# Kernel optimization log

Hardware: AMD Instinct MI355X
Metric: run time of the kernel (lower is better)

## Reference

```python
import jax, jax.numpy as jnp
import numpy as np

EPS = 1e-5

def _conv1x1(w, x):
    # w: [out,in], x: [b,in,h,w] -> [b,out,h,w]
    return jnp.einsum('oi,bihw->bohw', w, x)

def _aggregate(resp, persp, t_w, p_w, g_w, z_w, gamma, beta):
    t = _conv1x1(t_w, persp)                      # b,c,h,w
    b, c, h, w = t.shape
    tq = t.reshape(b, c, h * w).transpose(0, 2, 1)            # b,N,c
    p = _conv1x1(p_w, resp).reshape(b, c, -1)                 # b,c,M
    g = _conv1x1(g_w, resp).reshape(b, c, -1).transpose(0, 2, 1)  # b,M,c
    att = jax.nn.softmax(jnp.einsum('bnc,bcm->bnm', tq, p), axis=2)  # b,N,M
    out = jnp.einsum('bnm,bmc->bnc', att, g)                  # b,N,c
    # faithful to torch: .contiguous().view(b,c,h,w) with NO permute
    out = out.reshape(b, c, h, w)
    z = _conv1x1(z_w, out)                                    # b,Cp,h,w
    mean = z.mean(axis=(0, 2, 3), keepdims=True)
    var = z.var(axis=(0, 2, 3), keepdims=True)                # biased (train-mode BN)
    zn = (z - mean) / jnp.sqrt(var + EPS)
    return zn * gamma[None, :, None, None] + beta[None, :, None, None]

def setup_inputs() -> dict:
    key = jax.random.key(0)
    ks = jax.random.split(key, 32)
    Cp, Cr, planes = 256, [64, 256, 512, 1024, 2048], 64
    hw = [48, 48, 24, 12, 6]
    d = {}
    d['perspective'] = jax.random.normal(ks[0], (4, Cp, 48, 48), jnp.float32)
    for i in range(5):
        d[f'response{i}'] = jax.random.normal(ks[1 + i], (4, Cr[i], hw[i], hw[i]), jnp.float32)
    d['t_w'] = jax.random.normal(ks[6], (planes, Cp), jnp.float32) * 0.05
    d['z_w'] = jax.random.normal(ks[7], (Cp, planes), jnp.float32) * 0.05
    for i in range(5):
        d[f'p{i}_w'] = jax.random.normal(ks[8 + 2 * i], (planes, Cr[i]), jnp.float32) * 0.05
        d[f'g{i}_w'] = jax.random.normal(ks[9 + 2 * i], (planes, Cr[i]), jnp.float32) * 0.05
        d[f'bn{i}_g'] = jnp.ones((Cp,), jnp.float32)
        d[f'bn{i}_b'] = jnp.zeros((Cp,), jnp.float32)
    return d

def reference(perspective, response0, response1, response2, response3, response4,
              t_w, z_w,
              p0_w, g0_w, bn0_g, bn0_b,
              p1_w, g1_w, bn1_g, bn1_b,
              p2_w, g2_w, bn2_g, bn2_b,
              p3_w, g3_w, bn3_g, bn3_b,
              p4_w, g4_w, bn4_g, bn4_b):
    resps = [response0, response1, response2, response3, response4]
    ps = [p0_w, p1_w, p2_w, p3_w, p4_w]
    gs = [g0_w, g1_w, g2_w, g3_w, g4_w]
    gms = [bn0_g, bn1_g, bn2_g, bn3_g, bn4_g]
    bts = [bn0_b, bn1_b, bn2_b, bn3_b, bn4_b]
    out = None
    for i in range(5):
        o = _aggregate(resps[i], perspective, t_w, ps[i], gs[i], z_w, gms[i], bts[i])
        out = o if out is None else out + o
    return out
```

## Files before the change

kernel.cpp:

```cpp
#include <hip/hip_runtime.h>
#include <hip/hip_bf16.h>
#include <string.h>

#define BB 4
#define CPc 256
#define NN 2304

typedef __attribute__((ext_vector_type(8))) short bf16x8;
typedef __attribute__((ext_vector_type(4))) float f32x4;

__device__ __forceinline__ short f2b(float x) {
    __hip_bfloat16 h = __float2bfloat16(x);
    return *reinterpret_cast<short*>(&h);
}
__device__ __forceinline__ float b2f16(short v) {
    union { float f; unsigned u; } x;
    x.u = ((unsigned)(unsigned short)v) << 16;
    return x.f;
}

__global__ __launch_bounds__(256) void k_wcvt(
    const float* __restrict__ t_w, const float* __restrict__ z_w,
    const float* p0, const float* p1, const float* p2, const float* p3, const float* p4,
    const float* g0, const float* g1, const float* g2, const float* g3, const float* g4,
    short* __restrict__ TWb, short* __restrict__ ZWb,
    short* __restrict__ WPb, short* __restrict__ WGb) {
    int idx = blockIdx.x * 256 + threadIdx.x;
    if (idx < 16384) { TWb[idx] = f2b(t_w[idx]); return; }
    if (idx < 32768) { ZWb[idx - 16384] = f2b(z_w[idx - 16384]); return; }
    int k = idx - 32768;
    bool isP = k < 249856;
    if (!isP) k -= 249856;
    int i, off;
    if (k < 4096)        { i = 0; off = 0; }
    else if (k < 20480)  { i = 1; off = 4096; }
    else if (k < 53248)  { i = 2; off = 20480; }
    else if (k < 118784) { i = 3; off = 53248; }
    else                 { i = 4; off = 118784; }
    const float* s;
    if (isP) s = (i == 0) ? p0 : (i == 1) ? p1 : (i == 2) ? p2 : (i == 3) ? p3 : p4;
    else     s = (i == 0) ? g0 : (i == 1) ? g1 : (i == 2) ? g2 : (i == 3) ? g3 : g4;
    (isP ? WPb : WGb)[k] = f2b(s[k - off]);
}

__global__ __launch_bounds__(256) void k_conv(
    const float* __restrict__ persp,
    const float* r0, const float* r1, const float* r2, const float* r3, const float* r4,
    const short* __restrict__ TWb, const short* __restrict__ WPb, const short* __restrict__ WGb,
    short* __restrict__ TQb, short* __restrict__ PTb, short* __restrict__ GTb,
    float* __restrict__ PPART, float* __restrict__ GPART) {
    const int CUM[7]  = {0, 144, 288, 432, 504, 552, 584};
    const int CRs[6]  = {256, 64, 256, 512, 1024, 2048};
    const int Mus[6]  = {2304, 2304, 2304, 576, 144, 36};
    const int Mps[6]  = {2304, 2304, 2304, 576, 192, 64};
    const int KSs[6]  = {1, 1, 1, 2, 4, 8};
    const int WOFF[6] = {0, 0, 4096, 20480, 53248, 118784};
    const int POFF[6] = {0, 0, 589824, 1179648, 1327104, 1376256};
    const int PBASE[6] = {0, 0, 0, 0, 294912, 491520};

    __shared__ __align__(16) short s_a[64][72];

    int blk = blockIdx.x, t = threadIdx.x;
    int w = t >> 6, lane = t & 63, lo = lane & 15, quad = lane >> 4;
    int seg = 0;
#pragma unroll
    for (int s_ = 1; s_ <= 5; ++s_) if (blk >= CUM[s_]) seg = s_;
    int Cr = CRs[seg], M = Mus[seg], Mp = Mps[seg], KS = KSs[seg];
    const float* in = (seg == 0) ? persp : (seg == 1) ? r0 : (seg == 2) ? r1 :
                      (seg == 3) ? r2 : (seg == 4) ? r3 : r4;
    const short* wp = (seg == 0) ? TWb : WPb + WOFF[seg];
    const short* wg = WGb + WOFF[seg];
    bool has_g = (seg != 0);
    int local = blk - CUM[seg];
    int mt = Mp >> 6;
    int b = local / (mt * KS);
    int rem = local % (mt * KS);
    int m0 = (rem / KS) * 64;
    int ksi = rem % KS;
    int kLen = Cr / KS, k0 = ksi * kLen;

    int ml = t & 63;
    int ssw = (ml >> 3) & 7;
    bool mvalid = (m0 + ml) < M;
    const float* inB = in + ((size_t)b * Cr) * M + m0 + ml;

    int mrow = w * 16 + lo;
    int rsw = (mrow >> 3) & 7;

    f32x4 accP[4], accG[4];
#pragma unroll
    for (int ct = 0; ct < 4; ++ct) {
        accP[ct] = f32x4{0.f, 0.f, 0.f, 0.f};
        accG[ct] = f32x4{0.f, 0.f, 0.f, 0.f};
    }

    for (int kc = k0; kc < k0 + kLen; kc += 64) {
        __syncthreads();
#pragma unroll
        for (int r = 0; r < 8; ++r) {
            int kp = (t >> 6) + r * 4;
            int q = kp >> 2, l = kp & 3;
            float v0 = 0.f, v1 = 0.f;
            if (mvalid) {
                v0 = inB[(size_t)(kc + 2 * kp) * M];
                v1 = inB[(size_t)(kc + 2 * kp + 1) * M];
            }
            short2 pk; pk.x = f2b(v0); pk.y = f2b(v1);
            *(short2*)&s_a[ml][(q ^ ssw) * 8 + l * 2] = pk;
        }
        __syncthreads();
        const bf16x8 fr0 = *(const bf16x8*)&s_a[mrow][8 * (quad ^ rsw)];
        const bf16x8 fr1 = *(const bf16x8*)&s_a[mrow][8 * ((4 + quad) ^ rsw)];
#pragma unroll
        for (int ct = 0; ct < 4; ++ct) {
            const bf16x8 fp0 = *(const bf16x8*)&wp[(size_t)(ct * 16 + lo) * Cr + kc + quad * 8];
            const bf16x8 fp1 = *(const bf16x8*)&wp[(size_t)(ct * 16 + lo) * Cr + kc + 32 + quad * 8];
            accP[ct] = __builtin_amdgcn_mfma_f32_16x16x32_bf16(fr0, fp0, accP[ct], 0, 0, 0);
            accP[ct] = __builtin_amdgcn_mfma_f32_16x16x32_bf16(fr1, fp1, accP[ct], 0, 0, 0);
            if (has_g) {
                const bf16x8 fg0 = *(const bf16x8*)&wg[(size_t)(ct * 16 + lo) * Cr + kc + quad * 8];
                const bf16x8 fg1 = *(const bf16x8*)&wg[(size_t)(ct * 16 + lo) * Cr + kc + 32 + quad * 8];
                accG[ct] = __builtin_amdgcn_mfma_f32_16x16x32_bf16(fg0, fr0, accG[ct], 0, 0, 0);
                accG[ct] = __builtin_amdgcn_mfma_f32_16x16x32_bf16(fg1, fr1, accG[ct], 0, 0, 0);
            }
        }
    }
    if (KS == 1) {
        short* outP = (seg == 0) ? TQb : PTb + POFF[seg];
        short* outG = GTb + POFF[seg];
        int mP = m0 + w * 16 + quad * 4;
#pragma unroll
        for (int ct = 0; ct < 4; ++ct) {
            int c = ct * 16 + lo;
#pragma unroll
            for (int rg = 0; rg < 4; ++rg)
                outP[((size_t)b * Mp + mP + rg) * 64 + c] = f2b(accP[ct][rg]);
        }
        if (has_g) {
            int mG = m0 + w * 16 + lo;
#pragma unroll
            for (int ct = 0; ct < 4; ++ct) {
                int cG = ct * 16 + quad * 4;
#pragma unroll
                for (int rg = 0; rg < 4; ++rg)
                    outG[((size_t)b * 64 + cG + rg) * Mp + mG] = f2b(accG[ct][rg]);
            }
        }
    } else {
        int NP = 4 * Mp * 64;
        float* pp = PPART + PBASE[seg] + (size_t)ksi * NP;
        float* gp = GPART + PBASE[seg] + (size_t)ksi * NP;
        int mP = m0 + w * 16 + quad * 4;
#pragma unroll
        for (int ct = 0; ct < 4; ++ct) {
            int c = ct * 16 + lo;
#pragma unroll
            for (int rg = 0; rg < 4; ++rg)
                pp[((size_t)b * Mp + mP + rg) * 64 + c] = accP[ct][rg];
        }
        int mG = m0 + w * 16 + lo;
#pragma unroll
        for (int ct = 0; ct < 4; ++ct) {
            int cG = ct * 16 + quad * 4;
#pragma unroll
            for (int rg = 0; rg < 4; ++rg)
                gp[((size_t)b * 64 + cG + rg) * Mp + mG] = accG[ct][rg];
        }
    }
}

__global__ __launch_bounds__(256) void k_cvt(const float* __restrict__ PPART,
                                             const float* __restrict__ GPART,
                                             short* __restrict__ PTb, short* __restrict__ GTb) {
    const int EC[4]    = {0, 147456, 196608, 212992};
    const int KSv[3]   = {2, 4, 8};
    const int PBASEv[3] = {0, 294912, 491520};
    const int POFFv[3] = {1179648, 1327104, 1376256};
    int e = blockIdx.x * 256 + threadIdx.x;
    int sg = (e < EC[1]) ? 0 : (e < EC[2]) ? 1 : 2;
    int rem = e - EC[sg];
    int KS = KSv[sg];
    int NP = (sg == 0) ? 147456 : (sg == 1) ? 49152 : 16384;
    {
        const float* src = PPART + PBASEv[sg] + rem;
        float p = 0.f;
        for (int s = 0; s < KS; ++s) p += src[(size_t)s * NP];
        PTb[POFFv[sg] + rem] = f2b(p);
    }
    {
        const float* src = GPART + PBASEv[sg] + rem;
        float g = 0.f;
        for (int s = 0; s < KS; ++s) g += src[(size_t)s * NP];
        GTb[POFFv[sg] + rem] = f2b(g);
    }
}

__global__ __launch_bounds__(256) void k_attn(const short* __restrict__ tq,
                                              const short* __restrict__ PTb,
                                              const short* __restrict__ GTb,
                                              short* __restrict__ OUTb,
                                              float* __restrict__ PNUM,
                                              float* __restrict__ PL) {
    const int AM[5]    = {2304, 2304, 576, 144, 36};
    const int AMp[5]   = {2304, 2304, 576, 192, 64};
    const int APOFF[5] = {0, 589824, 1179648, 1327104, 1376256};

    __shared__ __align__(16) short s_P[2][32][72];
    __shared__ float s_l[4][32];

    int t = threadIdx.x;
    int bid = blockIdx.x;
    int seg, r, p;
    if (bid < 2304) { seg = bid / 1152; int wi = bid % 1152; p = wi / 288; r = wi % 288; }
    else            { int q = bid - 2304; seg = 2 + q / 288; r = q % 288; p = 0; }
    int b = r / 72;
    int n0 = (r % 72) * 32;
    int M = AM[seg], Mp = AMp[seg];
    const short* pT = PTb + APOFF[seg];
    const short* gT = GTb + APOFF[seg];

    int w = t >> 6, lane = t & 63, lo = lane & 15, quad = lane >> 4;
    bool domask = (M != Mp);
    bool split = (seg < 2);

    int nch_tot = Mp >> 6;
    int c0, c1;
    if (split) { c0 = p * 9; c1 = c0 + 9; }
    else       { c0 = 0; c1 = nch_tot; }

    const short* tqB = tq + ((size_t)b * NN + n0 + lo) * 64 + quad * 8;
    bf16x8 bq[2][2];
#pragma unroll
    for (int i = 0; i < 2; ++i)
#pragma unroll
        for (int h = 0; h < 2; ++h)
            bq[i][h] = *(const bf16x8*)(tqB + i * 16 * 64 + h * 32);

    const short* pA = pT + ((size_t)b * Mp + w * 16 + lo) * 64 + quad * 8;
    const short* gB = gT + ((size_t)b * 64 + w * 16 + lo) * Mp + quad * 8;

    size_t m00 = (size_t)c0 << 6;
    bf16x8 pa0 = *(const bf16x8*)(pA + m00 * 64);
    bf16x8 pa1 = *(const bf16x8*)(pA + m00 * 64 + 32);
    bf16x8 gb0 = *(const bf16x8*)(gB + m00);
    bf16x8 gb1 = *(const bf16x8*)(gB + m00 + 32);

    f32x4 accO[2];
    accO[0] = f32x4{0.f, 0.f, 0.f, 0.f};
    accO[1] = f32x4{0.f, 0.f, 0.f, 0.f};
    float lsum[2] = {0.f, 0.f};

    for (int ch = c0; ch < c1; ++ch) {
        int m0 = ch << 6;
        bf16x8 pa0n, pa1n, gb0n, gb1n;
        bool more = (ch + 1 < c1);
        if (more) {
            size_t mn = (size_t)(m0 + 64);
            pa0n = *(const bf16x8*)(pA + mn * 64);
            pa1n = *(const bf16x8*)(pA + mn * 64 + 32);
            gb0n = *(const bf16x8*)(gB + mn);
            gb1n = *(const bf16x8*)(gB + mn + 32);
        }
        f32x4 S[2];
        S[0] = f32x4{0.f, 0.f, 0.f, 0.f};
        S[0] = __builtin_amdgcn_mfma_f32_16x16x32_bf16(pa0, bq[0][0], S[0], 0, 0, 0);
        S[0] = __builtin_amdgcn_mfma_f32_16x16x32_bf16(pa1, bq[0][1], S[0], 0, 0, 0);
        S[1] = f32x4{0.f, 0.f, 0.f, 0.f};
        S[1] = __builtin_amdgcn_mfma_f32_16x16x32_bf16(pa0, bq[1][0], S[1], 0, 0, 0);
        S[1] = __builtin_amdgcn_mfma_f32_16x16x32_bf16(pa1, bq[1][1], S[1], 0, 0, 0);
        if (domask) {
#pragma unroll
            for (int rg = 0; rg < 4; ++rg) {
                bool oob = (m0 + w * 16 + quad * 4 + rg) >= M;
                if (oob) { S[0][rg] = -1e30f; S[1][rg] = -1e30f; }
            }
        }
        short (*sp)[72] = s_P[ch & 1];
#pragma unroll
        for (int i = 0; i < 2; ++i) {
            short4 pw;
#pragma unroll
            for (int rg = 0; rg < 4; ++rg) {
                float e = __expf(S[i][rg] - 40.f);
                lsum[i] += e;
                ((short*)&pw)[rg] = f2b(e);
            }
            *(short4*)&sp[i * 16 + lo][w * 16 + quad * 4] = pw;
        }
        __syncthreads();
#pragma unroll
        for (int i = 0; i < 2; ++i) {
            const bf16x8 a0 = *(const bf16x8*)&sp[i * 16 + lo][quad * 8];
            const bf16x8 a1 = *(const bf16x8*)&sp[i * 16 + lo][32 + quad * 8];
            accO[i] = __builtin_amdgcn_mfma_f32_16x16x32_bf16(a0, gb0, accO[i], 0, 0, 0);
            accO[i] = __builtin_amdgcn_mfma_f32_16x16x32_bf16(a1, gb1, accO[i], 0, 0, 0);
        }
        if (more) { pa0 = pa0n; pa1 = pa1n; gb0 = gb0n; gb1 = gb1n; }
    }
#pragma unroll
    for (int i = 0; i < 2; ++i) {
        lsum[i] += __shfl_xor(lsum[i], 16, 64);
        lsum[i] += __shfl_xor(lsum[i], 32, 64);
    }
    if (quad == 0) { s_l[w][lo] = lsum[0]; s_l[w][16 + lo] = lsum[1]; }
    __syncthreads();
    if (split) {
        float* np = PNUM + ((size_t)((seg * 4 + p) * 288 + r)) * 2048;
        float* lp = PL + ((size_t)((seg * 4 + p) * 288 + r)) * 32;
#pragma unroll
        for (int i = 0; i < 2; ++i)
#pragma unroll
            for (int rg = 0; rg < 4; ++rg) {
                int n = i * 16 + quad * 4 + rg;
                np[n * 64 + w * 16 + lo] = accO[i][rg];
                if (w == 0 && lo == 0) {
                    float lt = s_l[0][n] + s_l[1][n] + s_l[2][n] + s_l[3][n];
                    lp[n] = lt;
                }
            }
    } else {
        short* outm = OUTb + (size_t)seg * 589824;
#pragma unroll
        for (int i = 0; i < 2; ++i)
#pragma unroll
            for (int rg = 0; rg < 4; ++rg) {
                int n = i * 16 + quad * 4 + rg;
                float lt = s_l[0][n] + s_l[1][n] + s_l[2][n] + s_l[3][n];
                outm[((size_t)b * NN + n0 + n) * 64 + w * 16 + lo] = f2b(accO[i][rg] / lt);
            }
    }
}

__global__ __launch_bounds__(256) void k_comb(const float* __restrict__ PNUM,
                                              const float* __restrict__ PL,
                                              short* __restrict__ OUTb) {
    int e4 = (blockIdx.x * 256 + threadIdx.x) * 4;
    int s = e4 / 589824;
    int rem = e4 % 589824;
    int r = rem / 2048;
    int off = rem % 2048;
    int n = off >> 6;
    float ax = 0.f, ay = 0.f, az = 0.f, aw = 0.f, l = 0.f;
#pragma unroll
    for (int pp = 0; pp < 4; ++pp) {
        size_t blkb = (size_t)((s * 4 + pp) * 288 + r);
        const float4 v = *(const float4*)&PNUM[blkb * 2048 + off];
        ax += v.x; ay += v.y; az += v.z; aw += v.w;
        l += PL[blkb * 32 + n];
    }
    short4 o;
    o.x = f2b(ax / l);
    o.y = f2b(ay / l);
    o.z = f2b(az / l);
    o.w = f2b(aw / l);
    *(short4*)&OUTb[e4] = o;
}

__global__ __launch_bounds__(256) void k_z(const short* __restrict__ OUTb,
                                           const short* __restrict__ ZWb,
                                           short* __restrict__ Zb,
                                           float* __restrict__ PART) {
    __shared__ __align__(16) short s_ut[64][72];
    int t = threadIdx.x;
    int seg = blockIdx.x / 144;
    int r = blockIdx.x % 144;
    int b = r / 36;
    int sp0 = (r % 36) * 64;
    const short* F = OUTb + (size_t)seg * 589824 + (size_t)b * 147456;
    short* z = Zb + (size_t)seg * 2359296 + (size_t)b * 589824;
    float* part = PART + (size_t)(seg * 144 + r) * 512;

    int w = t >> 6, lane = t & 63, lo = lane & 15, quad = lane >> 4;

    bf16x8 af[4][2];
#pragma unroll
    for (int qt = 0; qt < 4; ++qt)
#pragma unroll
        for (int h = 0; h < 2; ++h)
            af[qt][h] = *(const bf16x8*)&ZWb[(size_t)(w * 64 + qt * 16 + lo) * 64 + h * 32 + quad * 8];

#pragma unroll
    for (int rr = 0; rr < 4; ++rr) {
        int idx = t + rr * 256;
        int spl = idx & 63;
        int cp0 = (idx >> 6) << 2;
        short4 pk;
        pk.x = F[(size_t)(cp0 + 0) * 2304 + sp0 + spl];
        pk.y = F[(size_t)(cp0 + 1) * 2304 + sp0 + spl];
        pk.z = F[(size_t)(cp0 + 2) * 2304 + sp0 + spl];
        pk.w = F[(size_t)(cp0 + 3) * 2304 + sp0 + spl];
        *(short4*)&s_ut[spl][cp0] = pk;
    }
    __syncthreads();

    bf16x8 bfr[4][2];
#pragma unroll
    for (int st = 0; st < 4; ++st)
#pragma unroll
        for (int h = 0; h < 2; ++h)
            bfr[st][h] = *(const bf16x8*)&s_ut[st * 16 + lo][h * 32 + quad * 8];

    f32x4 acc[4][4];
#pragma unroll
    for (int qt = 0; qt < 4; ++qt)
#pragma unroll
        for (int st = 0; st < 4; ++st) {
            acc[qt][st] = f32x4{0.f, 0.f, 0.f, 0.f};
            acc[qt][st] = __builtin_amdgcn_mfma_f32_16x16x32_bf16(af[qt][0], bfr[st][0], acc[qt][st], 0, 0, 0);
            acc[qt][st] = __builtin_amdgcn_mfma_f32_16x16x32_bf16(af[qt][1], bfr[st][1], acc[qt][st], 0, 0, 0);
        }

#pragma unroll
    for (int qt = 0; qt < 4; ++qt) {
        float s1[4] = {0.f, 0.f, 0.f, 0.f};
        float s2[4] = {0.f, 0.f, 0.f, 0.f};
        int qb = w * 64 + qt * 16 + quad * 4;
#pragma unroll
        for (int st = 0; st < 4; ++st) {
            int sp = sp0 + st * 16 + lo;
#pragma unroll
            for (int rg = 0; rg < 4; ++rg) {
                float v = acc[qt][st][rg];
                z[(size_t)(qb + rg) * 2304 + sp] = f2b(v);
                s1[rg] += v;
                s2[rg] += v * v;
            }
        }
#pragma unroll
        for (int rg = 0; rg < 4; ++rg) {
            for (int o = 8; o >= 1; o >>= 1) {
                s1[rg] += __shfl_xor(s1[rg], o, 16);
                s2[rg] += __shfl_xor(s2[rg], o, 16);
            }
            if (lo == 0) {
                float2 v2; v2.x = s1[rg]; v2.y = s2[rg];
                *(float2*)&part[(size_t)(qb + rg) * 2] = v2;
            }
        }
    }
}

__global__ __launch_bounds__(256) void k_stats(const float* __restrict__ PART,
                                               float* __restrict__ STATS) {
    int seg = blockIdx.x;
    int q = threadIdx.x;
    const float* p = PART + (size_t)seg * 144 * 512 + q * 2;
    float s1 = 0.f, s2 = 0.f;
#pragma unroll 16
    for (int blk = 0; blk < 144; ++blk) {
        float2 v = *(const float2*)&p[(size_t)blk * 512];
        s1 += v.x; s2 += v.y;
    }
    STATS[seg * 512 + q * 2] = s1;
    STATS[seg * 512 + q * 2 + 1] = s2;
}

__global__ __launch_bounds__(256) void k_final(
    const short* __restrict__ Zb, const float* __restrict__ STATS,
    const float* g0, const float* g1, const float* g2, const float* g3, const float* g4,
    const float* b0, const float* b1, const float* b2, const float* b3, const float* b4,
    float* __restrict__ outp) {
    int idx4 = (blockIdx.x * 256 + threadIdx.x) * 4;
    int q = (idx4 / NN) & 255;
    const float inv = 1.f / (float)(BB * NN);
    float4 o = {0.f, 0.f, 0.f, 0.f};
#pragma unroll
    for (int i = 0; i < 5; ++i) {
        float mean = STATS[i * 512 + q * 2] * inv;
        float var = STATS[i * 512 + q * 2 + 1] * inv - mean * mean;
        float rr = rsqrtf(var + 1e-5f);
        const float* gm = (i == 0) ? g0 : (i == 1) ? g1 : (i == 2) ? g2 : (i == 3) ? g3 : g4;
        const float* bt = (i == 0) ? b0 : (i == 1) ? b1 : (i == 2) ? b2 : (i == 3) ? b3 : b4;
        float sc = rr * gm[q];
        float ofs = bt[q] - mean * sc;
        short4 zv = *(const short4*)&Zb[(size_t)i * 2359296 + idx4];
        o.x += b2f16(zv.x) * sc + ofs;
        o.y += b2f16(zv.y) * sc + ofs;
        o.z += b2f16(zv.z) * sc + ofs;
        o.w += b2f16(zv.w) * sc + ofs;
    }
    *(float4*)&outp[idx4] = o;
}

extern "C" void kernel_launch(void* const* d_in, const int* in_sizes, int n_in,
                              void* d_out, int out_size, void* d_ws, size_t ws_size,
                              hipStream_t stream) {
    const float* persp = (const float*)d_in[0];
    const float* resp[5];
    for (int i = 0; i < 5; ++i) resp[i] = (const float*)d_in[1 + i];
    const float* t_w = (const float*)d_in[6];
    const float* z_w = (const float*)d_in[7];
    const float *p_w[5], *g_w[5], *bng[5], *bnb[5];
    for (int i = 0; i < 5; ++i) {
        p_w[i] = (const float*)d_in[8 + 4 * i];
        g_w[i] = (const float*)d_in[9 + 4 * i];
        bng[i] = (const float*)d_in[10 + 4 * i];
        bnb[i] = (const float*)d_in[11 + 4 * i];
    }
    short* TQb = (short*)d_ws;
    short* TWb = TQb + 589824;
    short* ZWb = TWb + 16384;
    short* WPb = ZWb + 16384;
    short* WGb = WPb + 249856;
    short* PTb = WGb + 249856;
    short* GTb = PTb + 1392640;
    short* Zb  = GTb + 1392640;
    short* OUTb  = (short*)((float*)d_ws + 7852032);
    float* STATS = (float*)d_ws + 7852032 + 2949120;
    float* PPART = STATS + 2560;
    float* GPART = PPART + 622592;
    float* PNUM = (float*)Zb;
    float* PL   = PNUM + 4718592;

    k_wcvt<<<2080, 256, 0, stream>>>(t_w, z_w,
        p_w[0], p_w[1], p_w[2], p_w[3], p_w[4],
        g_w[0], g_w[1], g_w[2], g_w[3], g_w[4],
        TWb, ZWb, WPb, WGb);
    k_conv<<<584, 256, 0, stream>>>(persp,
        resp[0], resp[1], resp[2], resp[3], resp[4],
        TWb, WPb, WGb, TQb, PTb, GTb, PPART, GPART);
    k_cvt<<<832, 256, 0, stream>>>(PPART, GPART, PTb, GTb);
    k_attn<<<3168, 256, 0, stream>>>(TQb, PTb, GTb, OUTb, PNUM, PL);
    k_comb<<<1152, 256, 0, stream>>>(PNUM, PL, OUTb);
    k_z<<<720, 256, 0, stream>>>(OUTb, ZWb, Zb, PPART);
    k_stats<<<5, 256, 0, stream>>>(PPART, STATS);
    k_final<<<2304, 256, 0, stream>>>(Zb, STATS,
        bng[0], bng[1], bng[2], bng[3], bng[4],
        bnb[0], bnb[1], bnb[2], bnb[3], bnb[4],
        (float*)d_out);
}
```

Baseline: 244.2 us.

## Give each wave its own 32 query rows over the full key chunk in attention

The attention kernel now assigns each wave 32 query rows over all 64 keys and all 64 output channels of a chunk, instead of splitting keys and channels across the four waves of a 32-row block. This removes the per-chunk block-wide __syncthreads and the shared-memory row-sum reduction, since each wave keeps its P tile in private LDS and finishes its sums with shuffles. Blocks now cover 128 rows, so the grid shrinks by a factor of four, and the partial-result layout and combine indexing change to match. In exchange, each wave loads more P/G fragments per chunk with no software prefetch, which raises register pressure and leaves fewer blocks to spread across the GPU.

```diff
diff --git a/kernel.cpp b/kernel.cpp
--- a/kernel.cpp
+++ b/kernel.cpp
@@ -205,16 +205,15 @@
     const int AMp[5]   = {2304, 2304, 576, 192, 64};
     const int APOFF[5] = {0, 589824, 1179648, 1327104, 1376256};
 
-    __shared__ __align__(16) short s_P[2][32][72];
-    __shared__ float s_l[4][32];
+    __shared__ __align__(16) short s_P[4][32][72];
 
     int t = threadIdx.x;
     int bid = blockIdx.x;
     int seg, r, p;
-    if (bid < 2304) { seg = bid / 1152; int wi = bid % 1152; p = wi / 288; r = wi % 288; }
-    else            { int q = bid - 2304; seg = 2 + q / 288; r = q % 288; p = 0; }
-    int b = r / 72;
-    int n0 = (r % 72) * 32;
+    if (bid < 576) { seg = bid / 288; int wi = bid % 288; p = wi / 72; r = wi % 72; }
+    else           { int q = bid - 576; seg = 2 + q / 72; r = q % 72; p = 0; }
+    int b = r / 18;
+    int n0 = (r % 18) * 128;
     int M = AM[seg], Mp = AMp[seg];
     const short* pT = PTb + APOFF[seg];
     const short* gT = GTb + APOFF[seg];
@@ -222,13 +221,13 @@
     int w = t >> 6, lane = t & 63, lo = lane & 15, quad = lane >> 4;
     bool domask = (M != Mp);
     bool split = (seg < 2);
-
-    int nch_tot = Mp >> 6;
+    int n0w = n0 + w * 32;
+
     int c0, c1;
     if (split) { c0 = p * 9; c1 = c0 + 9; }
-    else       { c0 = 0; c1 = nch_tot; }
-
-    const short* tqB = tq + ((size_t)b * NN + n0 + lo) * 64 + quad * 8;
+    else       { c0 = 0; c1 = Mp >> 6; }
+
+    const short* tqB = tq + ((size_t)b * NN + n0w + lo) * 64 + quad * 8;
     bf16x8 bq[2][2];
 #pragma unroll
     for (int i = 0; i < 2; ++i)
@@ -236,97 +235,111 @@
         for (int h = 0; h < 2; ++h)
             bq[i][h] = *(const bf16x8*)(tqB + i * 16 * 64 + h * 32);
 
-    const short* pA = pT + ((size_t)b * Mp + w * 16 + lo) * 64 + quad * 8;
-    const short* gB = gT + ((size_t)b * 64 + w * 16 + lo) * Mp + quad * 8;
-
-    size_t m00 = (size_t)c0 << 6;
-    bf16x8 pa0 = *(const bf16x8*)(pA + m00 * 64);
-    bf16x8 pa1 = *(const bf16x8*)(pA + m00 * 64 + 32);
-    bf16x8 gb0 = *(const bf16x8*)(gB + m00);
-    bf16x8 gb1 = *(const bf16x8*)(gB + m00 + 32);
-
-    f32x4 accO[2];
-    accO[0] = f32x4{0.f, 0.f, 0.f, 0.f};
-    accO[1] = f32x4{0.f, 0.f, 0.f, 0.f};
+    const short* pBase = pT + ((size_t)b * Mp + lo) * 64 + quad * 8;
+    const short* gBase = gT + ((size_t)b * 64 + lo) * Mp + quad * 8;
+
+    f32x4 accO[2][4];
+#pragma unroll
+    for (int i = 0; i < 2; ++i)
+#pragma unroll
+        for (int cs = 0; cs < 4; ++cs)
+            accO[i][cs] = f32x4{0.f, 0.f, 0.f, 0.f};
     float lsum[2] = {0.f, 0.f};
+
+    short (*sp)[72] = s_P[w];
 
     for (int ch = c0; ch < c1; ++ch) {
         int m0 = ch << 6;
-        bf16x8 pa0n, pa1n, gb0n, gb1n;
-        bool more = (ch + 1 < c1);
-        if (more) {
-            size_t mn = (size_t)(m0 + 64);
-            pa0n = *(const bf16x8*)(pA + mn * 64);
-            pa1n = *(const bf16x8*)(pA + mn * 64 + 32);
-            gb0n = *(const bf16x8*)(gB + mn);
-            gb1n = *(const bf16x8*)(gB + mn + 32);
-        }
-        f32x4 S[2];
-        S[0] = f32x4{0.f, 0.f, 0.f, 0.f};
-        S[0] = __builtin_amdgcn_mfma_f32_16x16x32_bf16(pa0, bq[0][0], S[0], 0, 0, 0);
-        S[0] = __builtin_amdgcn_mfma_f32_16x16x32_bf16(pa1, bq[0][1], S[0], 0, 0, 0);
-        S[1] = f32x4{0.f, 0.f, 0.f, 0.f};
-        S[1] = __builtin_amdgcn_mfma_f32_16x16x32_bf16(pa0, bq[1][0], S[1], 0, 0, 0);
-        S[1] = __builtin_amdgcn_mfma_f32_16x16x32_bf16(pa1, bq[1][1], S[1], 0, 0, 0);
+        bf16x8 pa[4][2];
+#pragma unroll
+        for (int ms = 0; ms < 4; ++ms)
+#pragma unroll
+            for (int h = 0; h < 2; ++h)
+                pa[ms][h] = *(const bf16x8*)(pBase + (size_t)(m0 + ms * 16) * 64 + h * 32);
+        bf16x8 gb[4][2];
+#pragma unroll
+        for (int cs = 0; cs < 4; ++cs)
+#pragma unroll
+            for (int h = 0; h < 2; ++h)
+                gb[cs][h] = *(const bf16x8*)(gBase + (size_t)(cs * 16) * Mp + m0 + h * 32);
+
+        f32x4 S[2][4];
+#pragma unroll
+        for (int i = 0; i < 2; ++i)
+#pragma unroll
+            for (int ms = 0; ms < 4; ++ms) {
+                S[i][ms] = f32x4{0.f, 0.f, 0.f, 0.f};
+                S[i][ms] = __builtin_amdgcn_mfma_f32_16x16x32_bf16(pa[ms][0], bq[i][0], S[i][ms], 0, 0, 0);
+                S[i][ms] = __builtin_amdgcn_mfma_f32_16x16x32_bf16(pa[ms][1], bq[i][1], S[i][ms], 0, 0, 0);
+            }
         if (domask) {
 #pragma unroll
-            for (int rg = 0; rg < 4; ++rg) {
-                bool oob = (m0 + w * 16 + quad * 4 + rg) >= M;
-                if (oob) { S[0][rg] = -1e30f; S[1][rg] = -1e30f; }
-            }
-        }
-        short (*sp)[72] = s_P[ch & 1];
-#pragma unroll
-        for (int i = 0; i < 2; ++i) {
-            short4 pw;
-#pragma unroll
-            for (int rg = 0; rg < 4; ++rg) {
-                float e = __expf(S[i][rg] - 40.f);
-                lsum[i] += e;
-                ((short*)&pw)[rg] = f2b(e);
-            }
-            *(short4*)&sp[i * 16 + lo][w * 16 + quad * 4] = pw;
-        }
-        __syncthreads();
-#pragma unroll
-        for (int i = 0; i < 2; ++i) {
-            const bf16x8 a0 = *(const bf16x8*)&sp[i * 16 + lo][quad * 8];
-            const bf16x8 a1 = *(const bf16x8*)&sp[i * 16 + lo][32 + quad * 8];
-            accO[i] = __builtin_amdgcn_mfma_f32_16x16x32_bf16(a0, gb0, accO[i], 0, 0, 0);
-            accO[i] = __builtin_amdgcn_mfma_f32_16x16x32_bf16(a1, gb1, accO[i], 0, 0, 0);
-        }
-        if (more) { pa0 = pa0n; pa1 = pa1n; gb0 = gb0n; gb1 = gb1n; }
+            for (int ms = 0; ms < 4; ++ms)
+#pragma unroll
+                for (int rg = 0; rg < 4; ++rg) {
+                    bool oob = (m0 + ms * 16 + quad * 4 + rg) >= M;
+                    if (oob) { S[0][ms][rg] = -1e30f; S[1][ms][rg] = -1e30f; }
+                }
+        }
+#pragma unroll
+        for (int i = 0; i < 2; ++i)
+#pragma unroll
+            for (int ms = 0; ms < 4; ++ms) {
+                short4 pw;
+#pragma unroll
+                for (int rg = 0; rg < 4; ++rg) {
+                    float e = __expf(S[i][ms][rg] - 40.f);
+                    lsum[i] += e;
+                    ((short*)&pw)[rg] = f2b(e);
+                }
+                *(short4*)&sp[i * 16 + lo][ms * 16 + quad * 4] = pw;
+            }
+        bf16x8 pf[2][2];
+#pragma unroll
+        for (int i = 0; i < 2; ++i)
+#pragma unroll
+            for (int h = 0; h < 2; ++h)
+                pf[i][h] = *(const bf16x8*)&sp[i * 16 + lo][h * 32 + quad * 8];
+#pragma unroll
+        for (int i = 0; i < 2; ++i)
+#pragma unroll
+            for (int cs = 0; cs < 4; ++cs) {
+                accO[i][cs] = __builtin_amdgcn_mfma_f32_16x16x32_bf16(pf[i][0], gb[cs][0], accO[i][cs], 0, 0, 0);
+                accO[i][cs] = __builtin_amdgcn_mfma_f32_16x16x32_bf16(pf[i][1], gb[cs][1], accO[i][cs], 0, 0, 0);
+            }
     }
 #pragma unroll
     for (int i = 0; i < 2; ++i) {
         lsum[i] += __shfl_xor(lsum[i], 16, 64);
         lsum[i] += __shfl_xor(lsum[i], 32, 64);
     }
-    if (quad == 0) { s_l[w][lo] = lsum[0]; s_l[w][16 + lo] = lsum[1]; }
-    __syncthreads();
     if (split) {
-        float* np = PNUM + ((size_t)((seg * 4 + p) * 288 + r)) * 2048;
-        float* lp = PL + ((size_t)((seg * 4 + p) * 288 + r)) * 32;
+        float* np = PNUM + ((size_t)((seg * 4 + p) * 72 + r)) * 8192;
+        float* lp = PL + ((size_t)((seg * 4 + p) * 72 + r)) * 128;
+        if (quad == 0) {
+            lp[w * 32 + lo] = lsum[0];
+            lp[w * 32 + 16 + lo] = lsum[1];
+        }
 #pragma unroll
         for (int i = 0; i < 2; ++i)
 #pragma unroll
-            for (int rg = 0; rg < 4; ++rg) {
-                int n = i * 16 + quad * 4 + rg;
-                np[n * 64 + w * 16 + lo] = accO[i][rg];
-                if (w == 0 && lo == 0) {
-                    float lt = s_l[0][n] + s_l[1][n] + s_l[2][n] + s_l[3][n];
-                    lp[n] = lt;
+            for (int cs = 0; cs < 4; ++cs)
+#pragma unroll
+                for (int rg = 0; rg < 4; ++rg) {
+                    int nl = w * 32 + i * 16 + quad * 4 + rg;
+                    np[nl * 64 + cs * 16 + lo] = accO[i][cs][rg];
                 }
-            }
     } else {
         short* outm = OUTb + (size_t)seg * 589824;
 #pragma unroll
         for (int i = 0; i < 2; ++i)
 #pragma unroll
             for (int rg = 0; rg < 4; ++rg) {
-                int n = i * 16 + quad * 4 + rg;
-                float lt = s_l[0][n] + s_l[1][n] + s_l[2][n] + s_l[3][n];
-                outm[((size_t)b * NN + n0 + n) * 64 + w * 16 + lo] = f2b(accO[i][rg] / lt);
+                float lt = __shfl(lsum[i], quad * 4 + rg, 64);
+                int n = n0w + i * 16 + quad * 4 + rg;
+#pragma unroll
+                for (int cs = 0; cs < 4; ++cs)
+                    outm[((size_t)b * NN + n) * 64 + cs * 16 + lo] = f2b(accO[i][cs][rg] / lt);
             }
     }
 }
@@ -337,16 +350,20 @@
     int e4 = (blockIdx.x * 256 + threadIdx.x) * 4;
     int s = e4 / 589824;
     int rem = e4 % 589824;
-    int r = rem / 2048;
-    int off = rem % 2048;
-    int n = off >> 6;
+    int row = rem / 64;
+    int c = rem % 64;
+    int b = row / 2304;
+    int ng = row % 2304;
+    int nblk = ng >> 7;
+    int nl = ng & 127;
+    int r = b * 18 + nblk;
     float ax = 0.f, ay = 0.f, az = 0.f, aw = 0.f, l = 0.f;
 #pragma unroll
     for (int pp = 0; pp < 4; ++pp) {
-        size_t blkb = (size_t)((s * 4 + pp) * 288 + r);
-        const float4 v = *(const float4*)&PNUM[blkb * 2048 + off];
+        size_t base = (size_t)((s * 4 + pp) * 72 + r);
+        const float4 v = *(const float4*)&PNUM[base * 8192 + nl * 64 + c];
         ax += v.x; ay += v.y; az += v.z; aw += v.w;
-        l += PL[blkb * 32 + n];
+        l += PL[base * 128 + nl];
     }
     short4 o;
     o.x = f2b(ax / l);
@@ -520,7 +537,7 @@
         resp[0], resp[1], resp[2], resp[3], resp[4],
         TWb, WPb, WGb, TQb, PTb, GTb, PPART, GPART);
     k_cvt<<<832, 256, 0, stream>>>(PPART, GPART, PTb, GTb);
-    k_attn<<<3168, 256, 0, stream>>>(TQb, PTb, GTb, OUTb, PNUM, PL);
+    k_attn<<<792, 256, 0, stream>>>(TQb, PTb, GTb, OUTb, PNUM, PL);
     k_comb<<<1152, 256, 0, stream>>>(PNUM, PL, OUTb);
     k_z<<<720, 256, 0, stream>>>(OUTb, ZWb, Zb, PPART);
     k_stats<<<5, 256, 0, stream>>>(PPART, STATS);
```

After: 243.8 us. No clear change (-0.1%).
